# Kernel tuning notes

Measured on AMD Instinct MI355X. Metric: run time of the kernel, lower is better.

The kernel has to match this reference:

```python
import jax, jax.numpy as jnp
import numpy as np

N_CODES = 1024
CODE_DIM = 256
DECAY = 0.99
EPS = 1e-05


def setup_inputs() -> dict:
    key = jax.random.key(0)
    k1, k2, k3, k4 = jax.random.split(key, 4)
    z = jax.random.normal(k1, (32, CODE_DIM, 32, 32), dtype=jnp.float32)
    embed = jax.random.normal(k2, (N_CODES, CODE_DIM), dtype=jnp.float32)
    cluster_size = jax.random.uniform(k3, (N_CODES,), dtype=jnp.float32)
    embed_avg = jax.random.normal(k4, (N_CODES, CODE_DIM), dtype=jnp.float32)
    return {"z": z, "embed": embed, "cluster_size": cluster_size, "embed_avg": embed_avg}


def reference(z, embed, cluster_size, embed_avg):
    B, D, H, W = z.shape
    K = embed.shape[0]
    # (B*H*W, D) tokens
    flat = jnp.transpose(z, (0, 2, 3, 1)).reshape(-1, D)
    distances = (
        jnp.sum(flat * flat, axis=1, keepdims=True)
        - 2.0 * flat @ embed.T
        + jnp.sum(embed * embed, axis=1)[None, :]
    )
    indices = jnp.argmin(distances, axis=1)  # (N,)
    z_q = embed[indices].reshape(B, H, W, D).transpose(0, 3, 1, 2)  # (B, D, H, W)

    # EMA codebook update (training mode), no onehot materialization
    cs = jax.ops.segment_sum(jnp.ones(flat.shape[0], dtype=flat.dtype), indices, num_segments=K)
    es = jax.ops.segment_sum(flat, indices, num_segments=K)
    new_cluster_size = cluster_size * DECAY + (1.0 - DECAY) * cs
    new_embed_avg = embed_avg * DECAY + (1.0 - DECAY) * es
    n = jnp.sum(new_cluster_size)
    cs_norm = (new_cluster_size + EPS) / (n + K * EPS) * n
    new_embed = new_embed_avg / cs_norm[:, None]

    # straight-through estimator
    z_q_st = z + jax.lax.stop_gradient(z_q - z)
    # torch: F.mse_loss(z.detach(), z_q) -> grads flow to z_q (codebook) only
    vq_loss = jnp.mean((jax.lax.stop_gradient(z) - z_q) ** 2)
    return (z_q_st, indices.reshape(B, H, W), vq_loss, new_embed, new_cluster_size, new_embed_avg)
```

## Files before the change

### kernel.cpp

```cpp
#include <hip/hip_runtime.h>
#include <stdint.h>

#define DECAY 0.99f
#define OMDECAY 0.01f
#define EPSV 1e-5f


typedef _Float16 half8 __attribute__((ext_vector_type(8)));
typedef float floatx4 __attribute__((ext_vector_type(4)));

typedef __attribute__((address_space(1))) const uint32_t gu32;
typedef __attribute__((address_space(3))) uint32_t lu32;

__device__ __forceinline__ void gld16(uint32_t* l, const uint32_t* g) {
    __builtin_amdgcn_global_load_lds((gu32*)g, (lu32*)l, 16, 0, 0);
}

__device__ __forceinline__ uint32_t pack_hl(float v) {
    _Float16 h = (_Float16)v;
    _Float16 lo = (_Float16)(v - (float)h);
    return (uint32_t)__builtin_bit_cast(unsigned short, h) |
           ((uint32_t)__builtin_bit_cast(unsigned short, lo) << 16);
}

__device__ __forceinline__ unsigned int encf(float s) {
    unsigned int b = __builtin_bit_cast(unsigned int, s);
    return (b & 0x80000000u) ? ~b : (b | 0x80000000u);
}
__device__ __forceinline__ float decf(unsigned int u) {
    unsigned int b = (u & 0x80000000u) ? (u ^ 0x80000000u) : ~u;
    return __builtin_bit_cast(float, b);
}

__global__ void prep_fused(const float* __restrict__ z,
                           uint32_t* __restrict__ A_hi32,
                           uint32_t* __restrict__ A_lo32,
                           const float* __restrict__ embed,
                           unsigned short* __restrict__ B_hi16,
                           unsigned short* __restrict__ B_lo16,
                           float* __restrict__ enorm,
                           float* __restrict__ cs ,
                           uint32_t* __restrict__ b64i,
                           float* __restrict__ znstash) {
    __shared__ uint32_t sp[32 * 258];
    __shared__ float znacc[4][32];
    const int bx = blockIdx.x;
    const int tid = threadIdx.x;
    const int lane = tid & 63;
    const int wv = tid >> 6;

    if (bx < 1024) {
        const int t0  = bx * 32;
        const int b   = t0 >> 10;
        const int hw0 = t0 & 1023;
        const int l32 = lane & 31;
        const int dh  = lane >> 5;
        float zn = 0.f;
        for (int dp = wv; dp < 128; dp += 4) {
            int dd = dp * 2 + dh;
            float v = z[b * 262144 + dd * 1024 + hw0 + l32];
            sp[l32 * 258 + dd] = pack_hl(v);
            zn += v * v;
        }
        zn += __shfl_xor(zn, 32);
        if (lane < 32) znacc[wv][lane] = zn;
        __syncthreads();
        if (tid < 32)
            znstash[t0 + tid] = znacc[0][tid] + znacc[1][tid] +
                                znacc[2][tid] + znacc[3][tid];
        for (int r = wv; r < 32; r += 4) {
#pragma unroll
            for (int h2 = 0; h2 < 2; ++h2) {
                int dpair = h2 * 64 + lane;
                uint32_t u0 = sp[r * 258 + 2 * dpair];
                uint32_t u1 = sp[r * 258 + 2 * dpair + 1];
                A_hi32[(t0 + r) * 128 + dpair] = (u0 & 0xffffu) | (u1 << 16);
                A_lo32[(t0 + r) * 128 + dpair] = (u0 >> 16) | (u1 & 0xffff0000u);
            }
        }
    } else {
        float* ws4 = (float*)sp;
        const int k = bx - 1024;
        const int d = tid;
        float v = embed[k * 256 + d];
        _Float16 h = (_Float16)v;
        _Float16 lo = (_Float16)(v - (float)h);
        const int c16 = k & 15, cg = k >> 4;
        const int dc = d >> 5, dl = d & 31;
        const int qq = dl >> 3, dw = (dl & 7) >> 1, hl = d & 1;
        const int us = ((cg * 8 + dc) * 256 + c16 * 16 + qq * 4 + dw) * 2 + hl;
        B_hi16[us] = __builtin_bit_cast(unsigned short, h);
        B_lo16[us] = __builtin_bit_cast(unsigned short, lo);
        float s = v * v;
        for (int off = 32; off > 0; off >>= 1) s += __shfl_down(s, off);
        if (lane == 0) ws4[wv] = s;
        __syncthreads();
        if (tid == 0) enorm[k] = ws4[0] + ws4[1] + ws4[2] + ws4[3];
        if (k < 256) b64i[k * 256 + tid] = 0xFFFFFFFFu;
        if (k == 0) {
            for (int i = tid; i < 2048; i += 256) cs[i] = 0.f;
        }
    }
}

__global__ __launch_bounds__(256, 2) void vq_mfma(
    const uint32_t* __restrict__ A_hi32,
    const uint32_t* __restrict__ A_lo32,
    const uint32_t* __restrict__ B_hi32,
    const uint32_t* __restrict__ B_lo32,
    const float* __restrict__ enorm,
    unsigned long long* __restrict__ best64)
{
    __shared__ __align__(16) _Float16 Abuf[2][2][4096];

    const int lane = threadIdx.x & 63;
    const int w    = threadIdx.x >> 6;
    const int q    = lane >> 4;
    const int c16  = lane & 15;
    const int bb   = blockIdx.x;
    const int xcd  = bb & 7;
    const int slot = bb >> 3;
    const int g    = (slot >> 2) * 8 + xcd;
    const int cq   = slot & 3;
    const int t0   = g * 128;
    const int cb   = cq * 256;
    const int lane4 = lane >> 2;
    const int dd8s  = ((lane & 3) ^ ((lane >> 3) & 3)) * 8;
    const int qs    = q ^ ((c16 >> 1) & 3);

    const uint32_t* const sA = (w >> 1) ? A_lo32 : A_hi32;
    const int r16b = (w & 1) * 4;

    float en[4];
    const uint32_t* bph[4];
    const uint32_t* bpl[4];
#pragma unroll
    for (int j = 0; j < 4; ++j) {
        const int code = cb + w * 64 + j * 16 + c16;
        en[j]  = enorm[code];
        const int cgj = (cb >> 4) + w * 4 + j;
        bph[j] = B_hi32 + cgj * 2048 + c16 * 16 + q * 4;
        bpl[j] = B_lo32 + cgj * 2048 + c16 * 16 + q * 4;
    }

    floatx4 acc[8][4];
#pragma unroll
    for (int i = 0; i < 8; ++i)
#pragma unroll
        for (int j = 0; j < 4; ++j)
            acc[i][j] = (floatx4){0.f, 0.f, 0.f, 0.f};

    half8 bh[2][4], bl[2][4];

    auto STAGE_A = [&](int step) {
        uint32_t* dst = (uint32_t*)(&Abuf[step & 1][w >> 1][0]);
        const int srcoff = (step * 32 + dd8s) >> 1;
#pragma unroll
        for (int s = 0; s < 4; ++s) {
            const int r16 = r16b + s;
            gld16(dst + r16 * 256, sA + (t0 + r16 * 16 + lane4) * 128 + srcoff);
        }
    };
    auto LOAD_B = [&](int step, half8* h, half8* l) {
#pragma unroll
        for (int j = 0; j < 4; ++j) {
            h[j] = *(const half8*)(bph[j] + step * 256);
            l[j] = *(const half8*)(bpl[j] + step * 256);
        }
    };

    STAGE_A(0);
    LOAD_B(0, bh[0], bl[0]);

#pragma unroll
    for (int dc = 0; dc < 8; ++dc) {
        if (dc < 7) {
            STAGE_A(dc + 1);
            LOAD_B(dc + 1, bh[(dc + 1) & 1], bl[(dc + 1) & 1]);
            asm volatile("s_waitcnt vmcnt(12)" ::: "memory");
        } else {
            asm volatile("s_waitcnt vmcnt(0)" ::: "memory");
        }
        __builtin_amdgcn_s_barrier();
        asm volatile("" ::: "memory");

        const _Float16* pH = &Abuf[dc & 1][0][0];
        const _Float16* pL = &Abuf[dc & 1][1][0];
        __builtin_amdgcn_s_setprio(1);
#pragma unroll
        for (int i = 0; i < 8; ++i) {
            const int off = (i * 16 + c16) * 32 + qs * 8;
            half8 aH = *(const half8*)(pH + off);
            half8 aL = *(const half8*)(pL + off);
#pragma unroll
            for (int j = 0; j < 4; ++j) {
                acc[i][j] = __builtin_amdgcn_mfma_f32_16x16x32_f16(aH, bh[dc & 1][j], acc[i][j], 0, 0, 0);
                acc[i][j] = __builtin_amdgcn_mfma_f32_16x16x32_f16(aH, bl[dc & 1][j], acc[i][j], 0, 0, 0);
                acc[i][j] = __builtin_amdgcn_mfma_f32_16x16x32_f16(aL, bh[dc & 1][j], acc[i][j], 0, 0, 0);
            }
        }
        __builtin_amdgcn_s_setprio(0);
        asm volatile("" ::: "memory");
        if (dc < 7) __builtin_amdgcn_s_barrier();
    }

    unsigned long long best[32];
#pragma unroll
    for (int sl = 0; sl < 32; ++sl) best[sl] = ~0ULL;
#pragma unroll
    for (int j = 0; j < 4; ++j) {
        const unsigned int code = (unsigned int)(cb + w * 64 + j * 16 + c16);
        const float enj = en[j];
#pragma unroll
        for (int i = 0; i < 8; ++i)
#pragma unroll
            for (int r = 0; r < 4; ++r) {
                float sc = enj - 2.0f * acc[i][j][r];
                unsigned long long key =
                    ((unsigned long long)encf(sc) << 32) | code;
                int sl = i * 4 + r;
                if (key < best[sl]) best[sl] = key;
            }
    }
#pragma unroll
    for (int sl = 0; sl < 32; ++sl) {
        unsigned long long v = best[sl];
#pragma unroll
        for (int mm = 1; mm < 16; mm <<= 1) {
            unsigned long long o = __shfl_xor(v, mm);
            if (o < v) v = o;
        }
        if (c16 == (sl & 15)) {
            int tok = t0 + (sl >> 2) * 16 + q * 4 + (sl & 3);
            atomicMin(&best64[tok], v);
        }
    }
}

__global__ __launch_bounds__(256) void merge_zq(
    const unsigned long long* __restrict__ best64,
    const float* __restrict__ embed,
    float* __restrict__ out_zq,
    float* __restrict__ out_idx ,
    float* __restrict__ cs,
    float* __restrict__ loss_sum)
{
    __shared__ int sidx[64];
    const int tid = threadIdx.x;
    const int lane = tid & 63;
    const int w = tid >> 6;
    const int t0 = blockIdx.x * 64;

    if (tid < 64) {
        unsigned long long key = best64[t0 + tid];
        int code = (int)(unsigned int)(key & 0xffffffffULL);
        float sc = decf((unsigned int)(key >> 32));
        float zn = out_idx[t0 + tid];
        sidx[tid] = code;
        out_idx[t0 + tid] = (float)code;
        atomicAdd(&cs[code], 1.0f);
        float val = zn + sc;
        for (int off = 32; off > 0; off >>= 1) val += __shfl_down(val, off);
        if (lane == 0) atomicAdd(loss_sum, val);
    }
    __syncthreads();

    const int b_idx = t0 >> 10;
    const int hw0   = t0 & 1023;
    const int zbase = b_idx * 262144 + hw0;
    const int ka = sidx[lane];
    const float* erow = embed + ka * 256;
    for (int dq = w; dq < 64; dq += 4) {
        float4 e4 = *(const float4*)(erow + dq * 4);
        out_zq[zbase + (dq * 4 + 0) * 1024 + lane] = e4.x;
        out_zq[zbase + (dq * 4 + 1) * 1024 + lane] = e4.y;
        out_zq[zbase + (dq * 4 + 2) * 1024 + lane] = e4.z;
        out_zq[zbase + (dq * 4 + 3) * 1024 + lane] = e4.w;
    }
}

__global__ void vq_finalize_small(const float* __restrict__ cluster_size,
                                  const float* __restrict__ cs,
                                  const float* __restrict__ loss_sum,
                                  float* __restrict__ out_loss,
                                  float* __restrict__ out_ncs,
                                  float* __restrict__ csnorm,
                                  int* __restrict__ offsets,
                                  int* __restrict__ cursor)
{
    __shared__ float wsum[16];
    __shared__ float wncs[16];
    __shared__ float stot[1];
    const int k = threadIdx.x;
    const int lane = k & 63;
    const int wv = k >> 6;
    float cnt = cs[k];
    float ncs = cluster_size[k] * DECAY + OMDECAY * cnt;
    out_ncs[k] = ncs;
    float sc = cnt;
#pragma unroll
    for (int d = 1; d < 64; d <<= 1) {
        float up = __shfl_up(sc, d);
        if (lane >= d) sc += up;
    }
    if (lane == 63) wsum[wv] = sc;
    float ns = ncs;
    for (int off = 32; off > 0; off >>= 1) ns += __shfl_down(ns, off);
    if (lane == 0) wncs[wv] = ns;
    __syncthreads();
    if (wv == 0) {
        float v = (lane < 16) ? wsum[lane] : 0.f;
#pragma unroll
        for (int d = 1; d < 16; d <<= 1) {
            float up = __shfl_up(v, d);
            if (lane >= d) v += up;
        }
        if (lane < 16) wsum[lane] = v;
    } else if (wv == 1) {
        float t = (lane < 16) ? wncs[lane] : 0.f;
        for (int off = 32; off > 0; off >>= 1) t += __shfl_down(t, off);
        if (lane == 0) stot[0] = t;
    }
    __syncthreads();
    float incl = sc + (wv ? wsum[wv - 1] : 0.f);
    int excl = __float2int_rn(incl - cnt);
    offsets[k] = excl;
    cursor[k]  = excl;
    float n = stot[0];
    csnorm[k] = (ncs + EPSV) / (n + 1024.0f * EPSV) * n;
    if (k == 0) out_loss[0] = loss_sum[0] / 8388608.0f;
}

__global__ void scatter_perm(const float* __restrict__ out_idx,
                             int* __restrict__ cursor,
                             int* __restrict__ perm,
                             float* __restrict__ es)
{
    int t = blockIdx.x * 256 + threadIdx.x;
#pragma unroll
    for (int i = 0; i < 8; ++i) es[t + i * 32768] = 0.f;
    int code = (int)out_idx[t];
    int pos = atomicAdd(&cursor[code], 1);
    perm[pos] = t;
}

__global__ void es_sum(const uint32_t* __restrict__ A_hi32,
                       const uint32_t* __restrict__ A_lo32,
                       const int* __restrict__ perm,
                       const float* __restrict__ out_idx,
                       float* __restrict__ es)
{
    __shared__ int sperm[32];
    __shared__ int scode[32];
    const int base = blockIdx.x * 32;
    const int tid = threadIdx.x;
    const int j = tid & 127;
    const uint32_t* __restrict__ A = (tid >> 7) ? A_lo32 : A_hi32;
    if (tid < 32) {
        int t = perm[base + tid];
        sperm[tid] = t;
        scode[tid] = (int)out_idx[t];
    }
    __syncthreads();

    float s0 = 0.f, s1 = 0.f;
    int cur = scode[0];
    uint32_t pu[2];
    pu[0] = A[sperm[0] * 128 + j];
    pu[1] = A[sperm[1] * 128 + j];
#pragma unroll
    for (int i = 0; i < 32; ++i) {
        uint32_t u = pu[i & 1];
        if (i + 2 < 32) pu[i & 1] = A[sperm[i + 2] * 128 + j];
        int code = scode[i];
        if (code != cur) {
            atomicAdd(&es[cur * 256 + 2 * j],     s0);
            atomicAdd(&es[cur * 256 + 2 * j + 1], s1);
            s0 = 0.f; s1 = 0.f; cur = code;
        }
        s0 += (float)__builtin_bit_cast(_Float16, (unsigned short)(u & 0xffffu));
        s1 += (float)__builtin_bit_cast(_Float16, (unsigned short)(u >> 16));
    }
    atomicAdd(&es[cur * 256 + 2 * j],     s0);
    atomicAdd(&es[cur * 256 + 2 * j + 1], s1);
}

__global__ void finalize_embed(const float* __restrict__ embed_avg,
                               const float* __restrict__ es,
                               const float* __restrict__ csnorm,
                               float* __restrict__ out_embed,
                               float* __restrict__ out_nea)
{
    int idx = blockIdx.x * 256 + threadIdx.x;
    int k = idx >> 8;
    float nea = embed_avg[idx] * DECAY + OMDECAY * es[idx];
    out_nea[idx] = nea;
    out_embed[idx] = nea / csnorm[k];
}

extern "C" void kernel_launch(void* const* d_in, const int* in_sizes, int n_in,
                              void* d_out, int out_size, void* d_ws, size_t ws_size,
                              hipStream_t stream) {
    const float* z            = (const float*)d_in[0];
    const float* embed        = (const float*)d_in[1];
    const float* cluster_size = (const float*)d_in[2];
    const float* embed_avg    = (const float*)d_in[3];
    float* out = (float*)d_out;
    uint32_t* ws32 = (uint32_t*)d_ws;

    uint32_t* B_hi32 = ws32 + 0;
    uint32_t* B_lo32 = ws32 + 131072;
    uint32_t* A_hi32 = ws32 + 262144;
    uint32_t* A_lo32 = ws32 + 4456448;
    int* perm        = (int*)(ws32 + 8650752);
    int* offsets     = (int*)(ws32 + 8683520);
    int* cursor      = (int*)(ws32 + 8684544);
    float* cs        = (float*)(ws32 + 8912896);
    float* loss_sum  = (float*)(ws32 + 8913920);
    float* enorm     = (float*)(ws32 + 8914944);
    float* csnorm    = (float*)(ws32 + 8915968);
    float* es        = (float*)(ws32 + 0);
    unsigned long long* best64 = (unsigned long long*)(out + 8421378);
    float* znstash = out + 8388608;

    prep_fused<<<2048, 256, 0, stream>>>(z, A_hi32, A_lo32, embed,
                                         (unsigned short*)B_hi32,
                                         (unsigned short*)B_lo32, enorm, cs,
                                         (uint32_t*)best64, znstash);
    vq_mfma<<<1024, 256, 0, stream>>>(A_hi32, A_lo32, B_hi32, B_lo32, enorm, best64);
    merge_zq<<<512, 256, 0, stream>>>(best64, embed,
                                      out, out + 8388608, cs, loss_sum);
    vq_finalize_small<<<1, 1024, 0, stream>>>(cluster_size, cs, loss_sum,
                                              out + 8421376, out + 8683521, csnorm,
                                              offsets, cursor);
    scatter_perm<<<128, 256, 0, stream>>>(out + 8388608, cursor, perm, es);
    es_sum<<<1024, 256, 0, stream>>>(A_hi32, A_lo32, perm, out + 8388608, es);
    finalize_embed<<<1024, 256, 0, stream>>>(embed_avg, es, csnorm,
                                             out + 8421377, out + 8684545);
}
```

Baseline: 230.5 us.

## Split the distance GEMM K-step into four phases interleaving loads and MFMAs

Restructures the main MFMA loop of the distance GEMM so each 32-wide K step runs as four phases. Each phase reads two A row-tiles from LDS, issues one slice of the next step's global B loads (plus the A staging in the first phase), syncs at a barrier, then runs its MFMAs at raised priority. The goal is to spread memory traffic across the compute instead of issuing all prefetches up front and stalling on them. The cost is four times as many barriers per step and a waitcnt that is now tuned by hand to the load order.

```diff
diff --git a/kernel.cpp b/kernel.cpp
--- a/kernel.cpp
+++ b/kernel.cpp
@@ -161,47 +161,59 @@
             gld16(dst + r16 * 256, sA + (t0 + r16 * 16 + lane4) * 128 + srcoff);
         }
     };
-    auto LOAD_B = [&](int step, half8* h, half8* l) {
-#pragma unroll
-        for (int j = 0; j < 4; ++j) {
-            h[j] = *(const half8*)(bph[j] + step * 256);
-            l[j] = *(const half8*)(bpl[j] + step * 256);
-        }
+    auto LOAD_B1 = [&](int step, int j, half8* h, half8* l) {
+        h[j] = *(const half8*)(bph[j] + step * 256);
+        l[j] = *(const half8*)(bpl[j] + step * 256);
     };
 
     STAGE_A(0);
-    LOAD_B(0, bh[0], bl[0]);
+#pragma unroll
+    for (int j = 0; j < 4; ++j) LOAD_B1(0, j, bh[0], bl[0]);
+    asm volatile("s_waitcnt vmcnt(8)" ::: "memory");
+    __builtin_amdgcn_s_barrier();
+    asm volatile("" ::: "memory");
 
 #pragma unroll
     for (int dc = 0; dc < 8; ++dc) {
-        if (dc < 7) {
-            STAGE_A(dc + 1);
-            LOAD_B(dc + 1, bh[(dc + 1) & 1], bl[(dc + 1) & 1]);
-            asm volatile("s_waitcnt vmcnt(12)" ::: "memory");
-        } else {
-            asm volatile("s_waitcnt vmcnt(0)" ::: "memory");
-        }
-        __builtin_amdgcn_s_barrier();
-        asm volatile("" ::: "memory");
-
-        const _Float16* pH = &Abuf[dc & 1][0][0];
-        const _Float16* pL = &Abuf[dc & 1][1][0];
-        __builtin_amdgcn_s_setprio(1);
-#pragma unroll
-        for (int i = 0; i < 8; ++i) {
-            const int off = (i * 16 + c16) * 32 + qs * 8;
-            half8 aH = *(const half8*)(pH + off);
-            half8 aL = *(const half8*)(pL + off);
-#pragma unroll
-            for (int j = 0; j < 4; ++j) {
-                acc[i][j] = __builtin_amdgcn_mfma_f32_16x16x32_f16(aH, bh[dc & 1][j], acc[i][j], 0, 0, 0);
-                acc[i][j] = __builtin_amdgcn_mfma_f32_16x16x32_f16(aH, bl[dc & 1][j], acc[i][j], 0, 0, 0);
-                acc[i][j] = __builtin_amdgcn_mfma_f32_16x16x32_f16(aL, bh[dc & 1][j], acc[i][j], 0, 0, 0);
-            }
-        }
-        __builtin_amdgcn_s_setprio(0);
-        asm volatile("" ::: "memory");
-        if (dc < 7) __builtin_amdgcn_s_barrier();
+        const int cur = dc & 1;
+        const int nxt = cur ^ 1;
+        const _Float16* pH = &Abuf[cur][0][0];
+        const _Float16* pL = &Abuf[cur][1][0];
+
+#pragma unroll
+        for (int ph = 0; ph < 4; ++ph) {
+            half8 aH[2], aL[2];
+#pragma unroll
+            for (int r = 0; r < 2; ++r) {
+                const int i = ph * 2 + r;
+                const int off = (i * 16 + c16) * 32 + qs * 8;
+                aH[r] = *(const half8*)(pH + off);
+                aL[r] = *(const half8*)(pL + off);
+            }
+            if (dc < 7) {
+                if (ph == 0) STAGE_A(dc + 1);
+                LOAD_B1(dc + 1, ph, bh[nxt], bl[nxt]);
+            }
+            __builtin_amdgcn_s_barrier();
+            asm volatile("" ::: "memory");
+            __builtin_amdgcn_s_setprio(1);
+#pragma unroll
+            for (int r = 0; r < 2; ++r) {
+                const int i = ph * 2 + r;
+#pragma unroll
+                for (int j = 0; j < 4; ++j) {
+                    acc[i][j] = __builtin_amdgcn_mfma_f32_16x16x32_f16(aH[r], bh[cur][j], acc[i][j], 0, 0, 0);
+                    acc[i][j] = __builtin_amdgcn_mfma_f32_16x16x32_f16(aH[r], bl[cur][j], acc[i][j], 0, 0, 0);
+                    acc[i][j] = __builtin_amdgcn_mfma_f32_16x16x32_f16(aL[r], bh[cur][j], acc[i][j], 0, 0, 0);
+                }
+            }
+            __builtin_amdgcn_s_setprio(0);
+            asm volatile("" ::: "memory");
+            if (ph == 3) {
+                asm volatile("s_waitcnt vmcnt(8)" ::: "memory");
+            }
+            __builtin_amdgcn_s_barrier();
+        }
     }
 
     unsigned long long best[32];
```

New measurement: 225.4 us. -2.2%, faster.

## Rework MFMA prefetch waits, stage gathered codebook rows in LDS, move es zeroing

Applied to the files above, without the earlier changes.

The distance kernel's main loop now waits on the next tile's loads after the compute step rather than before it, so global prefetch overlaps the MFMA work with one barrier per iteration. merge_zq first gathers the 64 selected codebook rows into padded shared memory with coalesced row reads, then writes the transposed z_q output from shared memory instead of doing strided per-lane float4 reads. Zeroing of the es accumulator moves from scatter_perm into merge_zq. The extra ~66KB of LDS per merge block may limit occupancy, and the reworked vmcnt counts must match the number of loads issued.

```diff
diff --git a/kernel.cpp b/kernel.cpp
--- a/kernel.cpp
+++ b/kernel.cpp
@@ -171,21 +171,19 @@
 
     STAGE_A(0);
     LOAD_B(0, bh[0], bl[0]);
+    asm volatile("s_waitcnt vmcnt(8)" ::: "memory");
+    __builtin_amdgcn_s_barrier();
+    asm volatile("" ::: "memory");
 
 #pragma unroll
     for (int dc = 0; dc < 8; ++dc) {
+        const int cur = dc & 1;
         if (dc < 7) {
             STAGE_A(dc + 1);
-            LOAD_B(dc + 1, bh[(dc + 1) & 1], bl[(dc + 1) & 1]);
-            asm volatile("s_waitcnt vmcnt(12)" ::: "memory");
-        } else {
-            asm volatile("s_waitcnt vmcnt(0)" ::: "memory");
-        }
-        __builtin_amdgcn_s_barrier();
-        asm volatile("" ::: "memory");
-
-        const _Float16* pH = &Abuf[dc & 1][0][0];
-        const _Float16* pL = &Abuf[dc & 1][1][0];
+            LOAD_B(dc + 1, bh[cur ^ 1], bl[cur ^ 1]);
+        }
+        const _Float16* pH = &Abuf[cur][0][0];
+        const _Float16* pL = &Abuf[cur][1][0];
         __builtin_amdgcn_s_setprio(1);
 #pragma unroll
         for (int i = 0; i < 8; ++i) {
@@ -194,14 +192,18 @@
             half8 aL = *(const half8*)(pL + off);
 #pragma unroll
             for (int j = 0; j < 4; ++j) {
-                acc[i][j] = __builtin_amdgcn_mfma_f32_16x16x32_f16(aH, bh[dc & 1][j], acc[i][j], 0, 0, 0);
-                acc[i][j] = __builtin_amdgcn_mfma_f32_16x16x32_f16(aH, bl[dc & 1][j], acc[i][j], 0, 0, 0);
-                acc[i][j] = __builtin_amdgcn_mfma_f32_16x16x32_f16(aL, bh[dc & 1][j], acc[i][j], 0, 0, 0);
+                acc[i][j] = __builtin_amdgcn_mfma_f32_16x16x32_f16(aH, bh[cur][j], acc[i][j], 0, 0, 0);
+                acc[i][j] = __builtin_amdgcn_mfma_f32_16x16x32_f16(aH, bl[cur][j], acc[i][j], 0, 0, 0);
+                acc[i][j] = __builtin_amdgcn_mfma_f32_16x16x32_f16(aL, bh[cur][j], acc[i][j], 0, 0, 0);
             }
         }
         __builtin_amdgcn_s_setprio(0);
         asm volatile("" ::: "memory");
-        if (dc < 7) __builtin_amdgcn_s_barrier();
+        if (dc < 7) {
+            asm volatile("s_waitcnt vmcnt(8)" ::: "memory");
+            __builtin_amdgcn_s_barrier();
+            asm volatile("" ::: "memory");
+        }
     }
 
     unsigned long long best[32];
@@ -243,13 +245,18 @@
     float* __restrict__ out_zq,
     float* __restrict__ out_idx ,
     float* __restrict__ cs,
-    float* __restrict__ loss_sum)
-{
+    float* __restrict__ loss_sum,
+    float* __restrict__ es)
+{
+    __shared__ float elds[64 * 257];
     __shared__ int sidx[64];
     const int tid = threadIdx.x;
     const int lane = tid & 63;
     const int w = tid >> 6;
     const int t0 = blockIdx.x * 64;
+
+    es[blockIdx.x * 512 + tid] = 0.f;
+    es[blockIdx.x * 512 + 256 + tid] = 0.f;
 
     if (tid < 64) {
         unsigned long long key = best64[t0 + tid];
@@ -265,17 +272,24 @@
     }
     __syncthreads();
 
+#pragma unroll
+    for (int k = 0; k < 16; ++k) {
+        const int row = w * 16 + k;
+        const int ka = sidx[row];
+        float4 v = *(const float4*)(embed + ka * 256 + lane * 4);
+        float* dst = elds + row * 257 + lane * 4;
+        dst[0] = v.x; dst[1] = v.y; dst[2] = v.z; dst[3] = v.w;
+    }
+    __syncthreads();
+
     const int b_idx = t0 >> 10;
     const int hw0   = t0 & 1023;
     const int zbase = b_idx * 262144 + hw0;
-    const int ka = sidx[lane];
-    const float* erow = embed + ka * 256;
-    for (int dq = w; dq < 64; dq += 4) {
-        float4 e4 = *(const float4*)(erow + dq * 4);
-        out_zq[zbase + (dq * 4 + 0) * 1024 + lane] = e4.x;
-        out_zq[zbase + (dq * 4 + 1) * 1024 + lane] = e4.y;
-        out_zq[zbase + (dq * 4 + 2) * 1024 + lane] = e4.z;
-        out_zq[zbase + (dq * 4 + 3) * 1024 + lane] = e4.w;
+    const float* src = elds + lane * 257;
+#pragma unroll
+    for (int dd = 0; dd < 64; ++dd) {
+        const int d = w * 64 + dd;
+        out_zq[zbase + d * 1024 + lane] = src[d];
     }
 }
 
@@ -333,12 +347,9 @@
 
 __global__ void scatter_perm(const float* __restrict__ out_idx,
                              int* __restrict__ cursor,
-                             int* __restrict__ perm,
-                             float* __restrict__ es)
+                             int* __restrict__ perm)
 {
     int t = blockIdx.x * 256 + threadIdx.x;
-#pragma unroll
-    for (int i = 0; i < 8; ++i) es[t + i * 32768] = 0.f;
     int code = (int)out_idx[t];
     int pos = atomicAdd(&cursor[code], 1);
     perm[pos] = t;
@@ -429,11 +440,11 @@
                                          (uint32_t*)best64, znstash);
     vq_mfma<<<1024, 256, 0, stream>>>(A_hi32, A_lo32, B_hi32, B_lo32, enorm, best64);
     merge_zq<<<512, 256, 0, stream>>>(best64, embed,
-                                      out, out + 8388608, cs, loss_sum);
+                                      out, out + 8388608, cs, loss_sum, es);
     vq_finalize_small<<<1, 1024, 0, stream>>>(cluster_size, cs, loss_sum,
                                               out + 8421376, out + 8683521, csnorm,
                                               offsets, cursor);
-    scatter_perm<<<128, 256, 0, stream>>>(out + 8388608, cursor, perm, es);
+    scatter_perm<<<128, 256, 0, stream>>>(out + 8388608, cursor, perm);
     es_sum<<<1024, 256, 0, stream>>>(A_hi32, A_lo32, perm, out + 8388608, es);
     finalize_embed<<<1024, 256, 0, stream>>>(embed_avg, es, csnorm,
                                              out + 8421377, out + 8684545);
```

Measured after the change: 226.0 us, median of 2. 1.02x faster.
